# Kernel tuning notes

Measured on AMD Instinct MI355X. Metric: run time of the kernel, lower is better.

## Reference

```python
import jax, jax.numpy as jnp
import numpy as np

ATTRACTION_W = 1.0
REPULSION_W = 1.0
BETA_POS_W = 1.0
BETA_NEG_W = 0.5
K_INST = 256  # max number of distinct instance ids (slice ids)


def setup_inputs() -> dict:
    key = jax.random.key(0)
    B, N, D, K = 4, 65536, 256, K_INST
    k1, k2, k3 = jax.random.split(key, 3)
    beta = jax.random.normal(k1, (B, N, 1), jnp.float32)
    embed = jax.random.normal(k2, (B, N, D), jnp.float32)
    sid = jax.random.randint(k3, (B, N), -1, K)  # -1 = background
    # force exactly one condensation point per instance: hit i (<K) -> sid=i, is_cp
    sid = sid.at[:, :K].set(jnp.broadcast_to(jnp.arange(K), (B, K)))
    is_cp = jnp.zeros((B, N), bool).at[:, :K].set(True)
    return {"beta": beta, "embed": embed, "slice_id": sid, "is_cp": is_cp}


def _loss_single(beta, emb, sid, cp):
    # beta: (N,) logits, emb: (N,D), sid: (N,) int, cp: (N,) bool
    N = sid.shape[0]
    valid = sid >= 0
    cpv = cp & valid  # condensation points with a valid instance id
    # BCE-with-logits: target 1 -> softplus(-x), target 0 -> softplus(x)
    pos = jnp.sum(jnp.where(cpv, jax.nn.softplus(-beta), 0.0)) / jnp.maximum(cpv.sum(), 1)
    noncp = ~cp
    neg = jnp.sum(jnp.where(noncp, jax.nn.softplus(beta), 0.0)) / jnp.maximum(noncp.sum(), 1)
    beta_loss = BETA_POS_W * pos + BETA_NEG_W * neg

    # first CP hit index per instance (segment-min over CP hits), N = "no CP"
    sid_c = jnp.where(valid, sid, 0)
    idx = jnp.arange(N)
    first_cp = jnp.full((K_INST,), N, jnp.int32).at[sid_c].min(
        jnp.where(cpv, idx, N).astype(jnp.int32))
    has_cp = first_cp < N
    cp_emb = emb[jnp.minimum(first_cp, N - 1)]  # (K, D), garbage where no CP

    # attraction: sum over instances of mean ||emb - inst_cp||^2
    d2 = jnp.sum((emb - cp_emb[sid_c]) ** 2, axis=-1)  # (N,)
    w = valid & has_cp[sid_c]
    seg_sum = jnp.zeros((K_INST,), jnp.float32).at[sid_c].add(jnp.where(w, d2, 0.0))
    seg_cnt = jnp.zeros((K_INST,), jnp.float32).at[sid_c].add(w.astype(jnp.float32))
    attraction = jnp.sum(jnp.where(seg_cnt > 0, seg_sum / jnp.maximum(seg_cnt, 1.0), 0.0))
    attraction = attraction * ATTRACTION_W

    # repulsion: mean exp(-||cp_i - cp_j||^2) over all CP pairs (incl. diagonal)
    pd2 = jnp.sum((cp_emb[:, None, :] - cp_emb[None, :, :]) ** 2, axis=-1)  # (K,K)
    pmask = has_cp[:, None] & has_cp[None, :]
    M = has_cp.sum()
    rep = jnp.sum(jnp.where(pmask, jnp.exp(-pd2), 0.0)) / jnp.maximum(M * M, 1)
    rep = jnp.where(M > 1, rep * REPULSION_W, 0.0)

    loss = beta_loss + attraction + rep
    ok = (valid.sum() > 0) & (cpv.sum() > 0)
    return jnp.where(ok, loss, 0.0), ok


def reference(beta, embed, slice_id, is_cp):
    losses, oks = jax.vmap(_loss_single)(beta.squeeze(-1), embed, slice_id, is_cp)
    cnt = oks.sum()
    return jnp.where(cnt > 0, losses.sum() / jnp.maximum(cnt, 1), 0.0)
```

## Files before the change

kernel.cpp:

```cpp
#include <hip/hip_runtime.h>
#include <math.h>

#define K_INST 256
#define ATTRACTION_W 1.0f
#define REPULSION_W 1.0f
#define BETA_POS_W 1.0f
#define BETA_NEG_W 0.5f

typedef float f32x4 __attribute__((ext_vector_type(4)));
typedef int i32x4 __attribute__((ext_vector_type(4)));

__device__ inline float softplusf(float x) {
    return fmaxf(x, 0.f) + log1pf(expf(-fabsf(x)));
}

__device__ inline float waveReduceSumF(float v) {
    for (int o = 32; o; o >>= 1) v += __shfl_xor(v, o);
    return v;
}
__device__ inline int waveReduceSumI(int v) {
    for (int o = 32; o; o >>= 1) v += __shfl_xor(v, o);
    return v;
}

__global__ void stats_kernel(const float* __restrict__ beta,
                             const int* __restrict__ sid,
                             const int* __restrict__ is_cp,
                             int* first_cp,
                             float* pos_sum, float* neg_sum,
                             int* cpv_cnt, int* noncp_cnt, int* valid_cnt,
                             int N) {
    int b = blockIdx.y;
    int base = (blockIdx.x * blockDim.x + threadIdx.x) * 4;
    const float* betaB = beta + (size_t)b * N;
    const int* sidB = sid + (size_t)b * N;
    const int* cpB = is_cp + (size_t)b * N;

    i32x4 s4 = *(const i32x4*)(sidB + base);
    i32x4 c4 = *(const i32x4*)(cpB + base);
    f32x4 x4 = *(const f32x4*)(betaB + base);

    float pos = 0.f, neg = 0.f;
    int c_cpv = 0, c_non = 0, c_val = 0;
    #pragma unroll
    for (int e = 0; e < 4; ++e) {
        int s = s4[e], cp = c4[e];
        float x = x4[e];
        bool valid = s >= 0;
        bool cpv = cp && valid;
        if (cpv) {
            pos += softplusf(-x);
            c_cpv++;
            atomicMin(&first_cp[b * K_INST + s], base + e);
        }
        if (!cp) {
            neg += softplusf(x);
            c_non++;
        }
        c_val += valid ? 1 : 0;
    }

    __shared__ float sf[2][4];
    __shared__ int si[3][4];
    pos = waveReduceSumF(pos);
    neg = waveReduceSumF(neg);
    c_cpv = waveReduceSumI(c_cpv);
    c_non = waveReduceSumI(c_non);
    c_val = waveReduceSumI(c_val);
    int wave = threadIdx.x >> 6, lane = threadIdx.x & 63;
    if (lane == 0) {
        sf[0][wave] = pos; sf[1][wave] = neg;
        si[0][wave] = c_cpv; si[1][wave] = c_non; si[2][wave] = c_val;
    }
    __syncthreads();
    if (threadIdx.x == 0) {
        float p = sf[0][0] + sf[0][1] + sf[0][2] + sf[0][3];
        float n = sf[1][0] + sf[1][1] + sf[1][2] + sf[1][3];
        int a = si[0][0] + si[0][1] + si[0][2] + si[0][3];
        int c = si[1][0] + si[1][1] + si[1][2] + si[1][3];
        int v = si[2][0] + si[2][1] + si[2][2] + si[2][3];
        if (p != 0.f) atomicAdd(&pos_sum[b], p);
        if (n != 0.f) atomicAdd(&neg_sum[b], n);
        if (a) atomicAdd(&cpv_cnt[b], a);
        if (c) atomicAdd(&noncp_cnt[b], c);
        if (v) atomicAdd(&valid_cnt[b], v);
    }
}

__global__ void gather_kernel(const float* __restrict__ embed,
                              const int* __restrict__ first_cp,
                              float* __restrict__ cp_emb,
                              float* __restrict__ cp_embT, int N) {
    int b = blockIdx.y;
    int k = blockIdx.x;
    int src = first_cp[b * K_INST + k];
    if (src >= N) src = N - 1;
    int lane = threadIdx.x;
    const float* embB = embed + (size_t)b * N * 256;
    f32x4 v = ((const f32x4*)(embB + (size_t)src * 256))[lane];
    ((f32x4*)(cp_emb + ((size_t)b * K_INST + k) * 256))[lane] = v;
    float* T = cp_embT + (size_t)b * K_INST * 256;
    int d = lane * 4;
    T[(size_t)(d + 0) * 256 + k] = v[0];
    T[(size_t)(d + 1) * 256 + k] = v[1];
    T[(size_t)(d + 2) * 256 + k] = v[2];
    T[(size_t)(d + 3) * 256 + k] = v[3];
}

__global__ void attraction_repulsion_kernel(
        const float* __restrict__ embed,
        const int* __restrict__ sid,
        const int* __restrict__ first_cp,
        const float* __restrict__ cp_emb,
        const float* __restrict__ cp_embT,
        float* seg_sum, int* seg_cnt, float* rep_sum,
        int N, int atr_blocks) {
    int b = blockIdx.y;
    __shared__ __align__(16) char smem[8448];
    __shared__ float sf[4];

    const float* cpB = cp_emb + (size_t)b * K_INST * 256;
    const int* fcB = first_cp + b * K_INST;

    if (blockIdx.x < 32) {
        float (*srow)[264] = (float(*)[264])smem;
        int i0 = blockIdx.x * 8;
        const float* T = cp_embT + (size_t)b * K_INST * 256;
        {
            int r = threadIdx.x >> 5, cc = (threadIdx.x & 31) * 8;
            f32x4 a = *(const f32x4*)(cpB + (size_t)(i0 + r) * 256 + cc);
            f32x4 bv = *(const f32x4*)(cpB + (size_t)(i0 + r) * 256 + cc + 4);
            srow[r][cc + 0] = a[0]; srow[r][cc + 1] = a[1];
            srow[r][cc + 2] = a[2]; srow[r][cc + 3] = a[3];
            srow[r][cc + 4] = bv[0]; srow[r][cc + 5] = bv[1];
            srow[r][cc + 6] = bv[2]; srow[r][cc + 7] = bv[3];
        }
        __syncthreads();

        int j = threadIdx.x;
        bool has_j = fcB[j] < N;
        float acc[8] = {0.f, 0.f, 0.f, 0.f, 0.f, 0.f, 0.f, 0.f};
        for (int d = 0; d < 256; d += 2) {
            float v0 = T[(size_t)d * 256 + j];
            float v1 = T[(size_t)(d + 1) * 256 + j];
            #pragma unroll
            for (int r = 0; r < 8; ++r) {
                float f0 = srow[r][d] - v0;
                float f1 = srow[r][d + 1] - v1;
                acc[r] += f0 * f0 + f1 * f1;
            }
        }
        float val = 0.f;
        #pragma unroll
        for (int r = 0; r < 8; ++r) {
            bool has_i = fcB[i0 + r] < N;
            if (has_i && has_j) val += expf(-acc[r]);
        }
        val = waveReduceSumF(val);
        int wave = threadIdx.x >> 6, lane = threadIdx.x & 63;
        if (lane == 0) sf[wave] = val;
        __syncthreads();
        if (threadIdx.x == 0)
            atomicAdd(&rep_sum[b], sf[0] + sf[1] + sf[2] + sf[3]);
    } else {
        float* s_sum = (float*)smem;
        int* s_cnt = (int*)(smem + 1024);
        for (int k = threadIdx.x; k < K_INST; k += blockDim.x) { s_sum[k] = 0.f; s_cnt[k] = 0; }
        __syncthreads();

        int bx = blockIdx.x - 32;
        int lane = threadIdx.x & 63;
        int wid = bx * 4 + (threadIdx.x >> 6);
        int stride = atr_blocks * 4 * 8;

        const float* embB = embed + (size_t)b * N * 256;
        const int* sidB = sid + (size_t)b * N;

        int i = wid * 8;
        i32x4 sa = {0, 0, 0, 0}, sb = {0, 0, 0, 0};
        if (i < N) {
            sa = __builtin_nontemporal_load((const i32x4*)(sidB + i));
            sb = __builtin_nontemporal_load((const i32x4*)(sidB + i + 4));
        }
        while (i < N) {
            int ss[8] = {sa[0], sa[1], sa[2], sa[3], sb[0], sb[1], sb[2], sb[3]};

            f32x4 e[8];
            #pragma unroll
            for (int j = 0; j < 8; ++j)
                e[j] = __builtin_nontemporal_load(
                    (const f32x4*)(embB + (size_t)(i + j) * 256 + lane * 4));
            f32x4 c[8];
            #pragma unroll
            for (int j = 0; j < 8; ++j) {
                int sc = ss[j] < 0 ? 0 : ss[j];
                c[j] = *(const f32x4*)(cpB + (size_t)sc * 256 + lane * 4);
            }
            int inext = i + stride;
            i32x4 na = {0, 0, 0, 0}, nb = {0, 0, 0, 0};
            if (inext < N) {
                na = __builtin_nontemporal_load((const i32x4*)(sidB + inext));
                nb = __builtin_nontemporal_load((const i32x4*)(sidB + inext + 4));
            }

            float v[8];
            #pragma unroll
            for (int j = 0; j < 8; ++j) {
                float d0 = e[j][0] - c[j][0], d1 = e[j][1] - c[j][1];
                float d2 = e[j][2] - c[j][2], d3 = e[j][3] - c[j][3];
                v[j] = d0 * d0 + d1 * d1 + d2 * d2 + d3 * d3;
            }
            #pragma unroll
            for (int j = 0; j < 8; ++j) v[j] = waveReduceSumF(v[j]);
            if (lane == 0) {
                #pragma unroll
                for (int j = 0; j < 8; ++j) {
                    if (ss[j] >= 0) {
                        atomicAdd(&s_sum[ss[j]], v[j]);
                        atomicAdd(&s_cnt[ss[j]], 1);
                    }
                }
            }
            sa = na; sb = nb;
            i = inext;
        }
        __syncthreads();
        for (int k = threadIdx.x; k < K_INST; k += blockDim.x) {
            if (s_cnt[k]) {
                atomicAdd(&seg_sum[b * K_INST + k], s_sum[k]);
                atomicAdd(&seg_cnt[b * K_INST + k], s_cnt[k]);
            }
        }
    }
}

__global__ void final_kernel(const int* __restrict__ first_cp,
                             const float* __restrict__ seg_sum,
                             const int* __restrict__ seg_cnt,
                             const float* __restrict__ pos_sum,
                             const float* __restrict__ neg_sum,
                             const float* __restrict__ rep_sum,
                             const int* __restrict__ cpv_cnt,
                             const int* __restrict__ noncp_cnt,
                             const int* __restrict__ valid_cnt,
                             float* out, int N, int B) {
    __shared__ float s_att[4];
    __shared__ int s_m[4];
    float loss_sum = 0.f;
    int ok_cnt = 0;
    int wave = threadIdx.x >> 6, lane = threadIdx.x & 63;
    for (int b = 0; b < B; ++b) {
        int k = threadIdx.x;
        int fc = first_cp[b * K_INST + k];
        int has = (fc < N) ? 1 : 0;
        int cnt = seg_cnt[b * K_INST + k];
        float att = (has && cnt > 0) ? (seg_sum[b * K_INST + k] / (float)cnt) : 0.f;
        att = waveReduceSumF(att);
        has = waveReduceSumI(has);
        if (lane == 0) { s_att[wave] = att; s_m[wave] = has; }
        __syncthreads();
        if (threadIdx.x == 0) {
            float attraction = (s_att[0] + s_att[1] + s_att[2] + s_att[3]) * ATTRACTION_W;
            int M = s_m[0] + s_m[1] + s_m[2] + s_m[3];
            float pos = pos_sum[b] / fmaxf((float)cpv_cnt[b], 1.f);
            float neg = neg_sum[b] / fmaxf((float)noncp_cnt[b], 1.f);
            float beta_loss = BETA_POS_W * pos + BETA_NEG_W * neg;
            float rep = 0.f;
            if (M > 1) {
                float mm = (float)M * (float)M;
                rep = (rep_sum[b] / fmaxf(mm, 1.f)) * REPULSION_W;
            }
            float loss = beta_loss + attraction + rep;
            bool ok = (valid_cnt[b] > 0) && (cpv_cnt[b] > 0);
            if (ok) { loss_sum += loss; ok_cnt += 1; }
        }
        __syncthreads();
    }
    if (threadIdx.x == 0) {
        out[0] = (ok_cnt > 0) ? (loss_sum / (float)ok_cnt) : 0.f;
    }
}

extern "C" void kernel_launch(void* const* d_in, const int* in_sizes, int n_in,
                              void* d_out, int out_size, void* d_ws, size_t ws_size,
                              hipStream_t stream) {
    const float* beta  = (const float*)d_in[0];
    const float* embed = (const float*)d_in[1];
    const int* sid     = (const int*)d_in[2];
    const int* is_cp   = (const int*)d_in[3];
    float* out = (float*)d_out;

    const int N = 65536;
    const int B = in_sizes[0] / N;
    (void)n_in; (void)out_size; (void)ws_size;

    char* ws = (char*)d_ws;
    int*   first_cp  = (int*)(ws + 0);
    float* seg_sum   = (float*)(ws + 4096);
    int*   seg_cnt   = (int*)(ws + 8192);
    float* pos_sum   = (float*)(ws + 12288);
    float* neg_sum   = (float*)(ws + 12352);
    float* rep_sum   = (float*)(ws + 12416);
    int*   cpv_cnt   = (int*)(ws + 12480);
    int*   noncp_cnt = (int*)(ws + 12544);
    int*   valid_cnt = (int*)(ws + 12608);
    float* cp_emb    = (float*)(ws + 16384);
    float* cp_embT   = (float*)(ws + 16384 + (size_t)B * K_INST * 256 * 4);

    hipMemsetAsync(first_cp, 0x7F, (size_t)B * K_INST * 4, stream);
    hipMemsetAsync(ws + 4096, 0, 12288, stream);

    stats_kernel<<<dim3(N / 1024, B), dim3(256), 0, stream>>>(
        beta, sid, is_cp, first_cp, pos_sum, neg_sum,
        cpv_cnt, noncp_cnt, valid_cnt, N);

    gather_kernel<<<dim3(K_INST, B), dim3(64), 0, stream>>>(
        embed, first_cp, cp_emb, cp_embT, N);

    const int atr_blocks = 512;
    attraction_repulsion_kernel<<<dim3(32 + atr_blocks, B), dim3(256), 0, stream>>>(
        embed, sid, first_cp, cp_emb, cp_embT,
        seg_sum, seg_cnt, rep_sum, N, atr_blocks);

    final_kernel<<<dim3(1), dim3(256), 0, stream>>>(
        first_cp, seg_sum, seg_cnt, pos_sum, neg_sum, rep_sum,
        cpv_cnt, noncp_cnt, valid_cnt, out, N, B);
}
```

Before: 98.70 us.

## Restructure attraction pass to quarter-wave per point with direct global atomics

The per-instance count histogram moves into the stats kernel, built with a shared-memory histogram and then flushed to global. The attraction kernel drops its grid-stride loop and its shared segment accumulators. Each wave now handles 4 points at a time, with 16 lanes per point and a 4-step shuffle reduction, and adds each point's distance straight into a global segment sum with an atomic. The 32 repulsion blocks now do attraction work as well, so both run in one grid. This aims to cut shuffle-reduction depth and loop overhead and to balance work across blocks. The cost is many more contended global float atomics on only 256 addresses per batch.

New measurement: 221.8 us. 125% more time.

```diff
diff --git a/kernel.cpp b/kernel.cpp
--- a/kernel.cpp
+++ b/kernel.cpp
@@ -28,6 +28,7 @@
                              const int* __restrict__ is_cp,
                              int* first_cp,
                              float* pos_sum, float* neg_sum,
+                             int* seg_cnt,
                              int* cpv_cnt, int* noncp_cnt, int* valid_cnt,
                              int N) {
     int b = blockIdx.y;
@@ -35,6 +36,10 @@
     const float* betaB = beta + (size_t)b * N;
     const int* sidB = sid + (size_t)b * N;
     const int* cpB = is_cp + (size_t)b * N;
+
+    __shared__ int hist[K_INST];
+    for (int k = threadIdx.x; k < K_INST; k += blockDim.x) hist[k] = 0;
+    __syncthreads();
 
     i32x4 s4 = *(const i32x4*)(sidB + base);
     i32x4 c4 = *(const i32x4*)(cpB + base);
@@ -48,6 +53,7 @@
         float x = x4[e];
         bool valid = s >= 0;
         bool cpv = cp && valid;
+        if (valid) atomicAdd(&hist[s], 1);
         if (cpv) {
             pos += softplusf(-x);
             c_cpv++;
@@ -84,6 +90,10 @@
         if (a) atomicAdd(&cpv_cnt[b], a);
         if (c) atomicAdd(&noncp_cnt[b], c);
         if (v) atomicAdd(&valid_cnt[b], v);
+    }
+    for (int k = threadIdx.x; k < K_INST; k += blockDim.x) {
+        int h = hist[k];
+        if (h) atomicAdd(&seg_cnt[b * K_INST + k], h);
     }
 }
 
@@ -113,23 +123,56 @@
         const int* __restrict__ first_cp,
         const float* __restrict__ cp_emb,
         const float* __restrict__ cp_embT,
-        float* seg_sum, int* seg_cnt, float* rep_sum,
-        int N, int atr_blocks) {
+        float* seg_sum, float* rep_sum, int N) {
     int b = blockIdx.y;
-    __shared__ __align__(16) char smem[8448];
-    __shared__ float sf[4];
-
-    const float* cpB = cp_emb + (size_t)b * K_INST * 256;
-    const int* fcB = first_cp + b * K_INST;
+    int lane = threadIdx.x & 63;
+    int wave = threadIdx.x >> 6;
+    int qw = lane >> 4;
+    int p  = lane & 15;
+
+    const float* embB = embed + (size_t)b * N * 256;
+    const float* cpB  = cp_emb + (size_t)b * K_INST * 256;
+    const int* sidB   = sid + (size_t)b * N;
+    float* segB       = seg_sum + b * K_INST;
+
+    int wid = blockIdx.x * 4 + wave;
+    int i0 = wid * 32;
+
+    #pragma unroll 2
+    for (int g = 0; g < 8; ++g) {
+        int ip = i0 + g * 4 + qw;
+        int s = sidB[ip];
+        int sc = s < 0 ? 0 : s;
+        const float* erow = embB + (size_t)ip * 256 + p * 4;
+        const float* crow = cpB + (size_t)sc * 256 + p * 4;
+        f32x4 e0 = __builtin_nontemporal_load((const f32x4*)(erow));
+        f32x4 e1 = __builtin_nontemporal_load((const f32x4*)(erow + 64));
+        f32x4 e2 = __builtin_nontemporal_load((const f32x4*)(erow + 128));
+        f32x4 e3 = __builtin_nontemporal_load((const f32x4*)(erow + 192));
+        f32x4 c0 = *(const f32x4*)(crow);
+        f32x4 c1 = *(const f32x4*)(crow + 64);
+        f32x4 c2 = *(const f32x4*)(crow + 128);
+        f32x4 c3 = *(const f32x4*)(crow + 192);
+        f32x4 d0 = e0 - c0, d1 = e1 - c1, d2 = e2 - c2, d3 = e3 - c3;
+        f32x4 acc = d0 * d0 + d1 * d1 + d2 * d2 + d3 * d3;
+        float v = acc[0] + acc[1] + acc[2] + acc[3];
+        v += __shfl_xor(v, 1);
+        v += __shfl_xor(v, 2);
+        v += __shfl_xor(v, 4);
+        v += __shfl_xor(v, 8);
+        if (p == 0 && s >= 0) atomicAdd(&segB[s], v);
+    }
 
     if (blockIdx.x < 32) {
-        float (*srow)[264] = (float(*)[264])smem;
-        int i0 = blockIdx.x * 8;
+        __shared__ float srow[8][264];
+        __shared__ float sf[4];
+        const int* fcB = first_cp + b * K_INST;
+        int i0r = blockIdx.x * 8;
         const float* T = cp_embT + (size_t)b * K_INST * 256;
         {
             int r = threadIdx.x >> 5, cc = (threadIdx.x & 31) * 8;
-            f32x4 a = *(const f32x4*)(cpB + (size_t)(i0 + r) * 256 + cc);
-            f32x4 bv = *(const f32x4*)(cpB + (size_t)(i0 + r) * 256 + cc + 4);
+            f32x4 a = *(const f32x4*)(cpB + (size_t)(i0r + r) * 256 + cc);
+            f32x4 bv = *(const f32x4*)(cpB + (size_t)(i0r + r) * 256 + cc + 4);
             srow[r][cc + 0] = a[0]; srow[r][cc + 1] = a[1];
             srow[r][cc + 2] = a[2]; srow[r][cc + 3] = a[3];
             srow[r][cc + 4] = bv[0]; srow[r][cc + 5] = bv[1];
@@ -153,84 +196,14 @@
         float val = 0.f;
         #pragma unroll
         for (int r = 0; r < 8; ++r) {
-            bool has_i = fcB[i0 + r] < N;
+            bool has_i = fcB[i0r + r] < N;
             if (has_i && has_j) val += expf(-acc[r]);
         }
         val = waveReduceSumF(val);
-        int wave = threadIdx.x >> 6, lane = threadIdx.x & 63;
         if (lane == 0) sf[wave] = val;
         __syncthreads();
         if (threadIdx.x == 0)
             atomicAdd(&rep_sum[b], sf[0] + sf[1] + sf[2] + sf[3]);
-    } else {
-        float* s_sum = (float*)smem;
-        int* s_cnt = (int*)(smem + 1024);
-        for (int k = threadIdx.x; k < K_INST; k += blockDim.x) { s_sum[k] = 0.f; s_cnt[k] = 0; }
-        __syncthreads();
-
-        int bx = blockIdx.x - 32;
-        int lane = threadIdx.x & 63;
-        int wid = bx * 4 + (threadIdx.x >> 6);
-        int stride = atr_blocks * 4 * 8;
-
-        const float* embB = embed + (size_t)b * N * 256;
-        const int* sidB = sid + (size_t)b * N;
-
-        int i = wid * 8;
-        i32x4 sa = {0, 0, 0, 0}, sb = {0, 0, 0, 0};
-        if (i < N) {
-            sa = __builtin_nontemporal_load((const i32x4*)(sidB + i));
-            sb = __builtin_nontemporal_load((const i32x4*)(sidB + i + 4));
-        }
-        while (i < N) {
-            int ss[8] = {sa[0], sa[1], sa[2], sa[3], sb[0], sb[1], sb[2], sb[3]};
-
-            f32x4 e[8];
-            #pragma unroll
-            for (int j = 0; j < 8; ++j)
-                e[j] = __builtin_nontemporal_load(
-                    (const f32x4*)(embB + (size_t)(i + j) * 256 + lane * 4));
-            f32x4 c[8];
-            #pragma unroll
-            for (int j = 0; j < 8; ++j) {
-                int sc = ss[j] < 0 ? 0 : ss[j];
-                c[j] = *(const f32x4*)(cpB + (size_t)sc * 256 + lane * 4);
-            }
-            int inext = i + stride;
-            i32x4 na = {0, 0, 0, 0}, nb = {0, 0, 0, 0};
-            if (inext < N) {
-                na = __builtin_nontemporal_load((const i32x4*)(sidB + inext));
-                nb = __builtin_nontemporal_load((const i32x4*)(sidB + inext + 4));
-            }
-
-            float v[8];
-            #pragma unroll
-            for (int j = 0; j < 8; ++j) {
-                float d0 = e[j][0] - c[j][0], d1 = e[j][1] - c[j][1];
-                float d2 = e[j][2] - c[j][2], d3 = e[j][3] - c[j][3];
-                v[j] = d0 * d0 + d1 * d1 + d2 * d2 + d3 * d3;
-            }
-            #pragma unroll
-            for (int j = 0; j < 8; ++j) v[j] = waveReduceSumF(v[j]);
-            if (lane == 0) {
-                #pragma unroll
-                for (int j = 0; j < 8; ++j) {
-                    if (ss[j] >= 0) {
-                        atomicAdd(&s_sum[ss[j]], v[j]);
-                        atomicAdd(&s_cnt[ss[j]], 1);
-                    }
-                }
-            }
-            sa = na; sb = nb;
-            i = inext;
-        }
-        __syncthreads();
-        for (int k = threadIdx.x; k < K_INST; k += blockDim.x) {
-            if (s_cnt[k]) {
-                atomicAdd(&seg_sum[b * K_INST + k], s_sum[k]);
-                atomicAdd(&seg_cnt[b * K_INST + k], s_cnt[k]);
-            }
-        }
     }
 }
 
@@ -311,16 +284,14 @@
     hipMemsetAsync(ws + 4096, 0, 12288, stream);
 
     stats_kernel<<<dim3(N / 1024, B), dim3(256), 0, stream>>>(
-        beta, sid, is_cp, first_cp, pos_sum, neg_sum,
+        beta, sid, is_cp, first_cp, pos_sum, neg_sum, seg_cnt,
         cpv_cnt, noncp_cnt, valid_cnt, N);
 
     gather_kernel<<<dim3(K_INST, B), dim3(64), 0, stream>>>(
         embed, first_cp, cp_emb, cp_embT, N);
 
-    const int atr_blocks = 512;
-    attraction_repulsion_kernel<<<dim3(32 + atr_blocks, B), dim3(256), 0, stream>>>(
-        embed, sid, first_cp, cp_emb, cp_embT,
-        seg_sum, seg_cnt, rep_sum, N, atr_blocks);
+    attraction_repulsion_kernel<<<dim3(512, B), dim3(256), 0, stream>>>(
+        embed, sid, first_cp, cp_emb, cp_embT, seg_sum, rep_sum, N);
 
     final_kernel<<<dim3(1), dim3(256), 0, stream>>>(
         first_cp, seg_sum, seg_cnt, pos_sum, neg_sum, rep_sum,
```

## Move segment counts to stats pass and use transposed butterfly reduction

Applied to the files above, without the earlier changes.

Per-instance counts are now built as a shared-memory histogram in the stats kernel, which removes the count atomics from the attraction loop. The eight per-wave distance sums are reduced together: three xor-shuffle steps over all eight values, a select so each lane keeps one, and three more shuffles. This replaces eight full six-step reductions and leaves eight lanes doing one atomic each instead of lane 0 doing sixteen serially. The attraction grid also shrinks from 512 to 480 blocks. The tradeoff is extra LDS atomics and a histogram flush in the stats kernel. Counts now include valid hits of instances without a CP, which the final kernel presumably masks via has_cp.

Measured after the change: 100.9 us. 1.02x slower.

```diff
diff --git a/kernel.cpp b/kernel.cpp
--- a/kernel.cpp
+++ b/kernel.cpp
@@ -28,6 +28,7 @@
                              const int* __restrict__ is_cp,
                              int* first_cp,
                              float* pos_sum, float* neg_sum,
+                             int* seg_cnt,
                              int* cpv_cnt, int* noncp_cnt, int* valid_cnt,
                              int N) {
     int b = blockIdx.y;
@@ -35,6 +36,10 @@
     const float* betaB = beta + (size_t)b * N;
     const int* sidB = sid + (size_t)b * N;
     const int* cpB = is_cp + (size_t)b * N;
+
+    __shared__ int hist[K_INST];
+    for (int k = threadIdx.x; k < K_INST; k += blockDim.x) hist[k] = 0;
+    __syncthreads();
 
     i32x4 s4 = *(const i32x4*)(sidB + base);
     i32x4 c4 = *(const i32x4*)(cpB + base);
@@ -48,6 +53,7 @@
         float x = x4[e];
         bool valid = s >= 0;
         bool cpv = cp && valid;
+        if (valid) atomicAdd(&hist[s], 1);
         if (cpv) {
             pos += softplusf(-x);
             c_cpv++;
@@ -84,6 +90,10 @@
         if (a) atomicAdd(&cpv_cnt[b], a);
         if (c) atomicAdd(&noncp_cnt[b], c);
         if (v) atomicAdd(&valid_cnt[b], v);
+    }
+    for (int k = threadIdx.x; k < K_INST; k += blockDim.x) {
+        int h = hist[k];
+        if (h) atomicAdd(&seg_cnt[b * K_INST + k], h);
     }
 }
 
@@ -107,13 +117,32 @@
     T[(size_t)(d + 3) * 256 + k] = v[3];
 }
 
+__device__ inline float sel8f(const float* v, int lane) {
+    float a0 = (lane & 1) ? v[1] : v[0];
+    float a1 = (lane & 1) ? v[3] : v[2];
+    float a2 = (lane & 1) ? v[5] : v[4];
+    float a3 = (lane & 1) ? v[7] : v[6];
+    float b0 = (lane & 2) ? a1 : a0;
+    float b1 = (lane & 2) ? a3 : a2;
+    return (lane & 4) ? b1 : b0;
+}
+__device__ inline int sel8i(const int* v, int lane) {
+    int a0 = (lane & 1) ? v[1] : v[0];
+    int a1 = (lane & 1) ? v[3] : v[2];
+    int a2 = (lane & 1) ? v[5] : v[4];
+    int a3 = (lane & 1) ? v[7] : v[6];
+    int b0 = (lane & 2) ? a1 : a0;
+    int b1 = (lane & 2) ? a3 : a2;
+    return (lane & 4) ? b1 : b0;
+}
+
 __global__ void attraction_repulsion_kernel(
         const float* __restrict__ embed,
         const int* __restrict__ sid,
         const int* __restrict__ first_cp,
         const float* __restrict__ cp_emb,
         const float* __restrict__ cp_embT,
-        float* seg_sum, int* seg_cnt, float* rep_sum,
+        float* seg_sum, float* rep_sum,
         int N, int atr_blocks) {
     int b = blockIdx.y;
     __shared__ __align__(16) char smem[8448];
@@ -164,8 +193,7 @@
             atomicAdd(&rep_sum[b], sf[0] + sf[1] + sf[2] + sf[3]);
     } else {
         float* s_sum = (float*)smem;
-        int* s_cnt = (int*)(smem + 1024);
-        for (int k = threadIdx.x; k < K_INST; k += blockDim.x) { s_sum[k] = 0.f; s_cnt[k] = 0; }
+        for (int k = threadIdx.x; k < K_INST; k += blockDim.x) s_sum[k] = 0.f;
         __syncthreads();
 
         int bx = blockIdx.x - 32;
@@ -211,25 +239,24 @@
                 v[j] = d0 * d0 + d1 * d1 + d2 * d2 + d3 * d3;
             }
             #pragma unroll
-            for (int j = 0; j < 8; ++j) v[j] = waveReduceSumF(v[j]);
-            if (lane == 0) {
+            for (int o = 1; o <= 4; o <<= 1) {
                 #pragma unroll
-                for (int j = 0; j < 8; ++j) {
-                    if (ss[j] >= 0) {
-                        atomicAdd(&s_sum[ss[j]], v[j]);
-                        atomicAdd(&s_cnt[ss[j]], 1);
-                    }
-                }
+                for (int j = 0; j < 8; ++j) v[j] += __shfl_xor(v[j], o);
+            }
+            float w = sel8f(v, lane & 7);
+            #pragma unroll
+            for (int o = 8; o <= 32; o <<= 1) w += __shfl_xor(w, o);
+            if (lane < 8) {
+                int s_sel = sel8i(ss, lane);
+                if (s_sel >= 0) atomicAdd(&s_sum[s_sel], w);
             }
             sa = na; sb = nb;
             i = inext;
         }
         __syncthreads();
         for (int k = threadIdx.x; k < K_INST; k += blockDim.x) {
-            if (s_cnt[k]) {
-                atomicAdd(&seg_sum[b * K_INST + k], s_sum[k]);
-                atomicAdd(&seg_cnt[b * K_INST + k], s_cnt[k]);
-            }
+            float v = s_sum[k];
+            if (v != 0.f) atomicAdd(&seg_sum[b * K_INST + k], v);
         }
     }
 }
@@ -311,16 +338,16 @@
     hipMemsetAsync(ws + 4096, 0, 12288, stream);
 
     stats_kernel<<<dim3(N / 1024, B), dim3(256), 0, stream>>>(
-        beta, sid, is_cp, first_cp, pos_sum, neg_sum,
+        beta, sid, is_cp, first_cp, pos_sum, neg_sum, seg_cnt,
         cpv_cnt, noncp_cnt, valid_cnt, N);
 
     gather_kernel<<<dim3(K_INST, B), dim3(64), 0, stream>>>(
         embed, first_cp, cp_emb, cp_embT, N);
 
-    const int atr_blocks = 512;
+    const int atr_blocks = 480;
     attraction_repulsion_kernel<<<dim3(32 + atr_blocks, B), dim3(256), 0, stream>>>(
         embed, sid, first_cp, cp_emb, cp_embT,
-        seg_sum, seg_cnt, rep_sum, N, atr_blocks);
+        seg_sum, rep_sum, N, atr_blocks);
 
     final_kernel<<<dim3(1), dim3(256), 0, stream>>>(
         first_cp, seg_sum, seg_cnt, pos_sum, neg_sum, rep_sum,
```
